# Kernel tuning notes

Hardware: AMD Instinct MI355X
Metric: run time of the kernel (lower is better)

## Reference

```python
import jax, jax.numpy as jnp
import numpy as np

SEQ, D_A, H, D_K, D_V = 4096, 2048, 16, 128, 128


def setup_inputs() -> dict:
    key = jax.random.key(0)
    ks = jax.random.split(key, 7)
    return {
        "queries": jax.random.normal(ks[0], (SEQ, D_A), dtype=jnp.float32),
        "keys":    jax.random.normal(ks[1], (SEQ, D_A), dtype=jnp.float32),
        "values":  jax.random.normal(ks[2], (SEQ, D_A), dtype=jnp.float32),
        "Eq": jax.random.normal(ks[3], (H, D_A, D_K), dtype=jnp.float32),
        "Ek": jax.random.normal(ks[4], (H, D_A, D_K), dtype=jnp.float32),
        "Ev": jax.random.normal(ks[5], (H, D_A, D_V), dtype=jnp.float32),
        "W_out": jax.random.normal(ks[6], (H * D_V, D_A), dtype=jnp.float32),
    }


def reference(queries, keys, values, Eq, Ek, Ev, W_out):
    # Per-head projections: [seq, d_a] x [h, d_a, d] -> [h, seq, d]
    Q = jnp.einsum("sd,hdk->hsk", queries, Eq)
    K = jnp.einsum("sd,hdk->hsk", keys, Ek)
    V = jnp.einsum("sd,hdv->hsv", values, Ev)
    scale = 1.0 / D_K  # faithful to source: 1/d_k, not 1/sqrt(d_k)
    dots = jnp.einsum("hqk,hsk->hqs", Q, K) * scale  # [h, seq, seq]
    attn = jax.nn.softmax(dots, axis=-1)  # dropout p=0 -> identity
    out = jnp.einsum("hqs,hsv->hqv", attn, V)  # [h, seq, d_v]
    # concat heads along last dim: [seq, h*d_v]
    A = jnp.transpose(out, (1, 0, 2)).reshape(SEQ, H * D_V)
    return A @ W_out  # [seq, d_a]
```

## Files before the change

kernel.cpp:

```cpp
#include <hip/hip_runtime.h>

typedef unsigned short u16;
typedef __attribute__((ext_vector_type(4)))  float  f32x4;
typedef __attribute__((ext_vector_type(16))) float  f32x16;
typedef __attribute__((ext_vector_type(4)))  float  float4v;
typedef __attribute__((ext_vector_type(4)))  unsigned short u16x4;
typedef __attribute__((ext_vector_type(8)))  unsigned short u16x8;
typedef __attribute__((ext_vector_type(8)))  short s16x8;
typedef __attribute__((ext_vector_type(4)))  unsigned int u32x4;

#define SEQ 4096
#define DA  2048
#define NH  16
#define DKV 128

__device__ __forceinline__ u16 f2bf(float f) {
    unsigned u = __builtin_bit_cast(unsigned, f);
    u += 0x7FFFu + ((u >> 16) & 1u);
    return (u16)(u >> 16);
}
__device__ __forceinline__ float bf2f(u16 h) {
    return __builtin_bit_cast(float, (unsigned)h << 16);
}
__device__ __forceinline__ f32x4 mfma16(u16x8 a, u16x8 b, f32x4 c) {
    return __builtin_amdgcn_mfma_f32_16x16x32_bf16(
        __builtin_bit_cast(s16x8, a), __builtin_bit_cast(s16x8, b), c, 0, 0, 0);
}
__device__ __forceinline__ f32x16 mfma32(u16x8 a, u16x8 b, f32x16 c) {
    return __builtin_amdgcn_mfma_f32_32x32x16_bf16(
        __builtin_bit_cast(s16x8, a), __builtin_bit_cast(s16x8, b), c, 0, 0, 0);
}
__device__ __forceinline__ unsigned cvtpk(float lo, float hi) {
    unsigned r;
    asm("v_cvt_pk_bf16_f32 %0, %1, %2" : "=v"(r) : "v"(lo), "v"(hi));
    return r;
}
__device__ __forceinline__ void gld16(const u16* g, u16* l) {
    __builtin_amdgcn_global_load_lds(
        (const __attribute__((address_space(1))) unsigned int*)g,
        (__attribute__((address_space(3))) unsigned int*)l, 16, 0, 0);
}
__device__ __forceinline__ char* ldsp(void* base, int row, int bcol, int rowbytes) {
    int off = row * rowbytes + bcol;
    off ^= (row & 7) << 4;
    return (char*)base + off;
}
__device__ __forceinline__ char* ldsp256(void* base, int row, int bcol) {
    int off = row * 256 + bcol;
    off ^= (row & 15) << 4;
    return (char*)base + off;
}

__global__ void transpose_split_k(const float* __restrict__ in, u16* __restrict__ oh,
                                  u16* __restrict__ ol, int R, int C) {
    __shared__ float tile[32][33];
    int b  = blockIdx.z;
    int r0 = blockIdx.x * 32, c0 = blockIdx.y * 32;
    const float* src = in + (size_t)b * R * C;
    int t = threadIdx.x;
    {
        int cl = t & 31, r = t >> 5;
        for (int i = 0; i < 4; ++i)
            tile[r + 8 * i][cl] = src[(size_t)(r0 + r + 8 * i) * C + (c0 + cl)];
    }
    __syncthreads();
    int rl = t & 31, c = t >> 5;
    size_t obase = (size_t)b * R * C;
    for (int i = 0; i < 4; ++i) {
        int cw = c + 8 * i;
        float x = tile[rl][cw];
        u16 h = f2bf(x);
        size_t o = obase + (size_t)(c0 + cw) * R + (r0 + rl);
        oh[o] = h;
        if (ol) ol[o] = f2bf(x - bf2f(h));
    }
}

__global__ void split_cvt_k(const float* __restrict__ in, u16* __restrict__ oh,
                            u16* __restrict__ ol, float scale, int n) {
    int stride = gridDim.x * 256 * 4;
    for (int i = (blockIdx.x * 256 + threadIdx.x) * 4; i < n; i += stride) {
        float4v v = *(const float4v*)(in + i);
        u16x4 hv, lv;
#pragma unroll
        for (int j = 0; j < 4; ++j) {
            float x = v[j] * scale;
            u16 hh = f2bf(x);
            hv[j] = hh;
            lv[j] = f2bf(x - bf2f(hh));
        }
        *(u16x4*)(oh + i) = hv;
        if (ol) *(u16x4*)(ol + i) = lv;
    }
}

template <int MODE>
__global__ void __launch_bounds__(256, 2) proj2_k(const u16* __restrict__ ASh,
                                                  const u16* __restrict__ ASl,
                                                  const u16* __restrict__ BTh,
                                                  const u16* __restrict__ BTl,
                                                  u16* __restrict__ Oh,
                                                  u16* __restrict__ Ol) {
    __shared__ u16 sAh[128 * 64];
    __shared__ u16 sBh[128 * 64];
    __shared__ u16 sAl[MODE ? 128 * 64 : 8];
    __shared__ u16 sBl[MODE ? 128 * 64 : 8];

    int t = threadIdx.x;
    int h = blockIdx.y;
    int bm0 = blockIdx.x * 128;
    int lane = t & 63, w = t >> 6, wr = w >> 1, wc = w & 1;
    int g = lane >> 4, c = lane & 15;

    int rin = lane >> 3;
    int cg  = (lane & 7) ^ rin;

    f32x4 acc[4][4] = {};

    for (int k0 = 0; k0 < DA; k0 += 64) {
        __syncthreads();
#pragma unroll
        for (int j = 0; j < 4; ++j) {
            int chunk = w * 4 + j;
            int r = chunk * 8 + rin;
            size_t ga = (size_t)(bm0 + r) * DA + k0 + cg * 8;
            size_t gb = ((size_t)h * 128 + r) * DA + k0 + cg * 8;
            gld16(ASh + ga, &sAh[chunk * 512]);
            gld16(BTh + gb, &sBh[chunk * 512]);
            if (MODE) {
                gld16(ASl + ga, &sAl[chunk * 512]);
                gld16(BTl + gb, &sBl[chunk * 512]);
            }
        }
        __syncthreads();

        for (int kc = 0; kc < 2; ++kc) {
            int kb = (kc * 32 + g * 8) * 2;
            u16x8 ah[4], al[4], bh[4], bl[4];
            for (int m = 0; m < 4; ++m) {
                int row = wr * 64 + m * 16 + c;
                ah[m] = *(u16x8*)ldsp(sAh, row, kb, 128);
                if (MODE) al[m] = *(u16x8*)ldsp(sAl, row, kb, 128);
            }
            for (int n = 0; n < 4; ++n) {
                int row = wc * 64 + n * 16 + c;
                bh[n] = *(u16x8*)ldsp(sBh, row, kb, 128);
                if (MODE) bl[n] = *(u16x8*)ldsp(sBl, row, kb, 128);
            }
            for (int m = 0; m < 4; ++m)
                for (int n = 0; n < 4; ++n) {
                    acc[m][n] = mfma16(ah[m], bh[n], acc[m][n]);
                    if (MODE) {
                        acc[m][n] = mfma16(ah[m], bl[n], acc[m][n]);
                        acc[m][n] = mfma16(al[m], bh[n], acc[m][n]);
                    }
                }
        }
    }

    for (int m = 0; m < 4; ++m)
        for (int n = 0; n < 4; ++n) {
            int col  = wc * 64 + n * 16 + c;
            int row0 = bm0 + wr * 64 + m * 16 + g * 4;
            if (MODE == 0) {
                u16x4 pv;
                for (int j = 0; j < 4; ++j) pv[j] = f2bf(acc[m][n][j]);
                *(u16x4*)(Oh + ((size_t)h * DKV + col) * SEQ + row0) = pv;
            } else {
                for (int j = 0; j < 4; ++j) {
                    float v = acc[m][n][j];
                    u16 hh = f2bf(v);
                    size_t o = ((size_t)h * SEQ + row0 + j) * DKV + col;
                    Oh[o] = hh;
                    Ol[o] = f2bf(v - bf2f(hh));
                }
            }
        }
}

__global__ void __launch_bounds__(512, 1) attn_k(const u16* __restrict__ QH,
                                                 const u16* __restrict__ QL,
                                                 const u16* __restrict__ KH,
                                                 const u16* __restrict__ KL,
                                                 const u16* __restrict__ VT,
                                                 u16* __restrict__ Abuf) {
    __shared__ u16 sKh[2][64 * 128];
    __shared__ u16 sKl[2][64 * 128];
    __shared__ u16 sV [2][64 * 128];

    int t = threadIdx.x, lane = t & 63, w = t >> 6;
    int bid = blockIdx.x;
    int h  = (bid & 7) + 8 * ((bid >> 3) & 1);
    int q0 = (bid >> 4) * 256;
    int c = lane & 31, hi = lane >> 5;
    int qrow = q0 + w * 32 + c;

    u16x8 qh[8], ql[8];
    {
        size_t base = ((size_t)h * SEQ + qrow) * DKV + hi * 8;
#pragma unroll
        for (int dc = 0; dc < 8; ++dc) {
            qh[dc] = *(const u16x8*)(QH + base + dc * 16);
            ql[dc] = *(const u16x8*)(QL + base + dc * 16);
        }
    }

    f32x16 o[4] = {};
    float mrun = -3e38f, lrun = 0.f;

    const size_t kroot = (size_t)h * SEQ * DKV;
    const size_t vroot = (size_t)h * DKV * SEQ;

    auto stage = [&](int kv, int b) {
        const u16* khp = KH + kroot + (size_t)kv * DKV;
        const u16* klp = KL + kroot + (size_t)kv * DKV;
        const u16* vtp = VT + vroot + kv;
#pragma unroll
        for (int j = 0; j < 2; ++j) {
            int ci = w * 2 + j;
            int rK = ci * 4 + (lane >> 4);
            int cK = (lane & 15) ^ (rK & 15);
            gld16(khp + rK * DKV + cK * 8, &sKh[b][ci * 512]);
            gld16(klp + rK * DKV + cK * 8, &sKl[b][ci * 512]);
            int vd = ((cK >> 3) << 6) + rK;
            gld16(vtp + (size_t)vd * SEQ + (cK & 7) * 8, &sV[b][ci * 512]);
        }
    };

    stage(0, 0);
    const int NT = SEQ / 64;
    for (int it = 0; it < NT; ++it) {
        int b = it & 1;
        __syncthreads();
        if (it + 1 < NT) stage((it + 1) * 64, b ^ 1);

        f32x16 s[2] = {};
        __builtin_amdgcn_s_setprio(1);
#pragma unroll
        for (int kt = 0; kt < 2; ++kt) {
#pragma unroll
            for (int dc = 0; dc < 8; ++dc) {
                u16x8 kh = *(u16x8*)ldsp256(sKh[b], kt * 32 + c, dc * 32 + hi * 16);
                u16x8 kl = *(u16x8*)ldsp256(sKl[b], kt * 32 + c, dc * 32 + hi * 16);
                s[kt] = mfma32(kh, qh[dc], s[kt]);
                s[kt] = mfma32(kl, qh[dc], s[kt]);
                s[kt] = mfma32(kh, ql[dc], s[kt]);
            }
        }
        __builtin_amdgcn_s_setprio(0);

        float vmax = s[0][0];
#pragma unroll
        for (int r = 1; r < 16; ++r) vmax = fmaxf(vmax, s[0][r]);
#pragma unroll
        for (int r = 0; r < 16; ++r) vmax = fmaxf(vmax, s[1][r]);
        vmax = fmaxf(vmax, __shfl_xor(vmax, 32));
        if (!__all(vmax <= mrun + 8.0f)) {
            float mnew = fmaxf(mrun, vmax);
            float corr = __expf(mrun - mnew);
            mrun = mnew;
            lrun *= corr;
#pragma unroll
            for (int vt = 0; vt < 4; ++vt)
#pragma unroll
                for (int r = 0; r < 16; ++r) o[vt][r] *= corr;
        }
        float rs = 0.f;
#pragma unroll
        for (int kt = 0; kt < 2; ++kt)
#pragma unroll
            for (int r = 0; r < 16; ++r) {
                float p = __expf(s[kt][r] - mrun);
                s[kt][r] = p;
                rs += p;
            }
        rs += __shfl_xor(rs, 32);
        lrun += rs;

#pragma unroll
        for (int kt = 0; kt < 2; ++kt) {
            unsigned wv[8], xw[8];
#pragma unroll
            for (int i = 0; i < 8; ++i) wv[i] = cvtpk(s[kt][2 * i], s[kt][2 * i + 1]);
#pragma unroll
            for (int i = 0; i < 8; ++i) xw[i] = (unsigned)__shfl_xor((int)wv[i], 32);
            __builtin_amdgcn_s_setprio(1);
#pragma unroll
            for (int kc = 0; kc < 2; ++kc) {
                u32x4 pw;
                pw[0] = hi ? xw[4 * kc + 2] : wv[4 * kc + 0];
                pw[1] = hi ? xw[4 * kc + 3] : wv[4 * kc + 1];
                pw[2] = hi ? wv[4 * kc + 2] : xw[4 * kc + 0];
                pw[3] = hi ? wv[4 * kc + 3] : xw[4 * kc + 1];
                u16x8 pf = __builtin_bit_cast(u16x8, pw);
#pragma unroll
                for (int vt = 0; vt < 4; ++vt) {
                    int v = vt * 32 + c;
                    u16x8 vf = *(u16x8*)ldsp256(sV[b], v & 63,
                                                ((v >> 6) << 7) + kt * 64 + kc * 32 + hi * 16);
                    o[vt] = mfma32(vf, pf, o[vt]);
                }
            }
            __builtin_amdgcn_s_setprio(0);
        }
    }

    float inv = 1.0f / lrun;
#pragma unroll
    for (int vt = 0; vt < 4; ++vt)
#pragma unroll
        for (int rg = 0; rg < 4; ++rg) {
            u16x4 pv;
#pragma unroll
            for (int j = 0; j < 4; ++j) pv[j] = f2bf(o[vt][rg * 4 + j] * inv);
            *(u16x4*)(Abuf + (size_t)qrow * (NH * DKV) + h * DKV + vt * 32 + rg * 8 + hi * 4) = pv;
        }
}

__global__ void __launch_bounds__(256, 2) gemm_out_k(const u16* __restrict__ Abuf,
                                                     const u16* __restrict__ WT,
                                                     float* __restrict__ out) {
    __shared__ u16 sA[128 * 64];
    __shared__ u16 sB[128 * 64];
    int t = threadIdx.x, lane = t & 63, w = t >> 6, wr = w >> 1, wc = w & 1;
    int g = lane >> 4, c = lane & 15;
    int bm0 = blockIdx.x * 128, bn0 = blockIdx.y * 128;
    int rin = lane >> 3;
    int cg  = (lane & 7) ^ rin;
    f32x4 acc[4][4] = {};

    for (int k0 = 0; k0 < DA; k0 += 64) {
        __syncthreads();
#pragma unroll
        for (int j = 0; j < 4; ++j) {
            int chunk = w * 4 + j;
            int r = chunk * 8 + rin;
            gld16(Abuf + (size_t)(bm0 + r) * DA + k0 + cg * 8, &sA[chunk * 512]);
            gld16(WT   + (size_t)(bn0 + r) * DA + k0 + cg * 8, &sB[chunk * 512]);
        }
        __syncthreads();

        for (int kc = 0; kc < 2; ++kc) {
            int kb = (kc * 32 + g * 8) * 2;
            u16x8 af[4], bfq[4];
            for (int m = 0; m < 4; ++m) af[m]  = *(u16x8*)ldsp(sA, wr * 64 + m * 16 + c, kb, 128);
            for (int n = 0; n < 4; ++n) bfq[n] = *(u16x8*)ldsp(sB, wc * 64 + n * 16 + c, kb, 128);
            for (int m = 0; m < 4; ++m)
                for (int n = 0; n < 4; ++n)
                    acc[m][n] = mfma16(af[m], bfq[n], acc[m][n]);
        }
    }
    for (int m = 0; m < 4; ++m)
        for (int n = 0; n < 4; ++n) {
            int row0 = bm0 + wr * 64 + m * 16 + g * 4;
            int col  = bn0 + wc * 64 + n * 16 + c;
            for (int j = 0; j < 4; ++j)
                out[(size_t)(row0 + j) * DA + col] = acc[m][n][j];
        }
}

extern "C" void kernel_launch(void* const* d_in, const int* in_sizes, int n_in,
                              void* d_out, int out_size, void* d_ws, size_t ws_size,
                              hipStream_t stream) {
    const float* queries = (const float*)d_in[0];
    const float* keys    = (const float*)d_in[1];
    const float* values  = (const float*)d_in[2];
    const float* Eq      = (const float*)d_in[3];
    const float* Ek      = (const float*)d_in[4];
    const float* Ev      = (const float*)d_in[5];
    const float* Wout    = (const float*)d_in[6];
    float* out = (float*)d_out;

    const size_t PROJ = (size_t)NH * SEQ * DKV;
    const size_t TSZ  = (size_t)DA * DA;
    const size_t ASZ  = (size_t)SEQ * DA;
    u16* p  = (u16*)d_ws;
    u16* QH = p; p += PROJ;
    u16* QL = p; p += PROJ;
    u16* KH = p; p += PROJ;
    u16* KL = p; p += PROJ;
    u16* VT = p; p += PROJ;
    u16* AB = p; p += (size_t)SEQ * NH * DKV;
    u16* TH = p; p += TSZ;
    u16* TL = p; p += TSZ;
    u16* Sh = p; p += ASZ;
    u16* Sl = p; p += ASZ;

    dim3 tgE(DA / 32, DKV / 32, NH);
    dim3 tgW(DA / 32, DA / 32, 1);
    dim3 pg(SEQ / 128, NH);
    const int NELEM = SEQ * DA;

    transpose_split_k<<<tgE, 256, 0, stream>>>(Eq, TH, TL, DA, DKV);
    split_cvt_k<<<2048, 256, 0, stream>>>(queries, Sh, Sl, 1.0f / 128.0f, NELEM);
    proj2_k<2><<<pg, 256, 0, stream>>>(Sh, Sl, TH, TL, QH, QL);
    transpose_split_k<<<tgE, 256, 0, stream>>>(Ek, TH, TL, DA, DKV);
    split_cvt_k<<<2048, 256, 0, stream>>>(keys, Sh, Sl, 1.0f, NELEM);
    proj2_k<1><<<pg, 256, 0, stream>>>(Sh, Sl, TH, TL, KH, KL);
    transpose_split_k<<<tgE, 256, 0, stream>>>(Ev, TH, nullptr, DA, DKV);
    split_cvt_k<<<2048, 256, 0, stream>>>(values, Sh, nullptr, 1.0f, NELEM);
    proj2_k<0><<<pg, 256, 0, stream>>>(Sh, nullptr, TH, nullptr, VT, nullptr);
    transpose_split_k<<<tgW, 256, 0, stream>>>(Wout, TH, nullptr, DA, DA);
    attn_k<<<dim3(SEQ / 256 * NH), 512, 0, stream>>>(QH, QL, KH, KL, VT, AB);
    gemm_out_k<<<dim3(SEQ / 128, DA / 128), 256, 0, stream>>>(AB, TH, out);
}
```

Baseline: 576.2 us.

## Double-buffer LDS tiles in projection and output GEMM kernels

Both the projection GEMM and the output GEMM now use two LDS buffers and issue the next tile's global-to-LDS loads before computing on the current tile. This overlaps memory latency with MFMA work and drops one barrier per iteration. In the projection kernel the K-step is halved to 32 so LDS use stays within budget, and a new 64-byte-row XOR swizzle is added to match. The cost is more loop iterations and barriers in the projection kernel. There is also a risk that the wait on the async global_load_lds is not explicit, so correctness depends on the compiler inserting the right waitcnt before the barrier.

```diff
diff --git a/kernel.cpp b/kernel.cpp
--- a/kernel.cpp
+++ b/kernel.cpp
@@ -48,6 +48,11 @@
 __device__ __forceinline__ char* ldsp256(void* base, int row, int bcol) {
     int off = row * 256 + bcol;
     off ^= (row & 15) << 4;
+    return (char*)base + off;
+}
+__device__ __forceinline__ char* ldsp64B(void* base, int row, int bcol) {
+    int off = row * 64 + bcol;
+    off ^= ((row ^ (row >> 2)) & 3) << 4;
     return (char*)base + off;
 }
 
@@ -101,10 +106,10 @@
                                                   const u16* __restrict__ BTl,
                                                   u16* __restrict__ Oh,
                                                   u16* __restrict__ Ol) {
-    __shared__ u16 sAh[128 * 64];
-    __shared__ u16 sBh[128 * 64];
-    __shared__ u16 sAl[MODE ? 128 * 64 : 8];
-    __shared__ u16 sBl[MODE ? 128 * 64 : 8];
+    __shared__ u16 sAh[2][128 * 32];
+    __shared__ u16 sBh[2][128 * 32];
+    __shared__ u16 sAl[2][MODE ? 128 * 32 : 8];
+    __shared__ u16 sBl[2][MODE ? 128 * 32 : 8];
 
     int t = threadIdx.x;
     int h = blockIdx.y;
@@ -112,50 +117,52 @@
     int lane = t & 63, w = t >> 6, wr = w >> 1, wc = w & 1;
     int g = lane >> 4, c = lane & 15;
 
-    int rin = lane >> 3;
-    int cg  = (lane & 7) ^ rin;
-
     f32x4 acc[4][4] = {};
 
-    for (int k0 = 0; k0 < DA; k0 += 64) {
-        __syncthreads();
-#pragma unroll
-        for (int j = 0; j < 4; ++j) {
-            int chunk = w * 4 + j;
-            int r = chunk * 8 + rin;
+    auto stage = [&](int k0, int b) {
+#pragma unroll
+        for (int j = 0; j < 2; ++j) {
+            int ci = w * 2 + j;
+            int r  = ci * 16 + (lane >> 2);
+            int cg = (lane & 3) ^ ((r ^ (r >> 2)) & 3);
             size_t ga = (size_t)(bm0 + r) * DA + k0 + cg * 8;
             size_t gb = ((size_t)h * 128 + r) * DA + k0 + cg * 8;
-            gld16(ASh + ga, &sAh[chunk * 512]);
-            gld16(BTh + gb, &sBh[chunk * 512]);
+            gld16(ASh + ga, &sAh[b][ci * 512]);
+            gld16(BTh + gb, &sBh[b][ci * 512]);
             if (MODE) {
-                gld16(ASl + ga, &sAl[chunk * 512]);
-                gld16(BTl + gb, &sBl[chunk * 512]);
-            }
-        }
+                gld16(ASl + ga, &sAl[b][ci * 512]);
+                gld16(BTl + gb, &sBl[b][ci * 512]);
+            }
+        }
+    };
+
+    stage(0, 0);
+    const int NK = DA / 32;
+    for (int ks = 0; ks < NK; ++ks) {
+        int b = ks & 1;
         __syncthreads();
-
-        for (int kc = 0; kc < 2; ++kc) {
-            int kb = (kc * 32 + g * 8) * 2;
-            u16x8 ah[4], al[4], bh[4], bl[4];
-            for (int m = 0; m < 4; ++m) {
-                int row = wr * 64 + m * 16 + c;
-                ah[m] = *(u16x8*)ldsp(sAh, row, kb, 128);
-                if (MODE) al[m] = *(u16x8*)ldsp(sAl, row, kb, 128);
-            }
+        if (ks + 1 < NK) stage((ks + 1) * 32, b ^ 1);
+
+        int kb = g * 16;
+        u16x8 ah[4], al[4], bh[4], bl[4];
+        for (int m = 0; m < 4; ++m) {
+            int row = wr * 64 + m * 16 + c;
+            ah[m] = *(u16x8*)ldsp64B(sAh[b], row, kb);
+            if (MODE) al[m] = *(u16x8*)ldsp64B(sAl[b], row, kb);
+        }
+        for (int n = 0; n < 4; ++n) {
+            int row = wc * 64 + n * 16 + c;
+            bh[n] = *(u16x8*)ldsp64B(sBh[b], row, kb);
+            if (MODE) bl[n] = *(u16x8*)ldsp64B(sBl[b], row, kb);
+        }
+        for (int m = 0; m < 4; ++m)
             for (int n = 0; n < 4; ++n) {
-                int row = wc * 64 + n * 16 + c;
-                bh[n] = *(u16x8*)ldsp(sBh, row, kb, 128);
-                if (MODE) bl[n] = *(u16x8*)ldsp(sBl, row, kb, 128);
-            }
-            for (int m = 0; m < 4; ++m)
-                for (int n = 0; n < 4; ++n) {
-                    acc[m][n] = mfma16(ah[m], bh[n], acc[m][n]);
-                    if (MODE) {
-                        acc[m][n] = mfma16(ah[m], bl[n], acc[m][n]);
-                        acc[m][n] = mfma16(al[m], bh[n], acc[m][n]);
-                    }
+                acc[m][n] = mfma16(ah[m], bh[n], acc[m][n]);
+                if (MODE) {
+                    acc[m][n] = mfma16(ah[m], bl[n], acc[m][n]);
+                    acc[m][n] = mfma16(al[m], bh[n], acc[m][n]);
                 }
-        }
+            }
     }
 
     for (int m = 0; m < 4; ++m)
@@ -320,8 +327,8 @@
 __global__ void __launch_bounds__(256, 2) gemm_out_k(const u16* __restrict__ Abuf,
                                                      const u16* __restrict__ WT,
                                                      float* __restrict__ out) {
-    __shared__ u16 sA[128 * 64];
-    __shared__ u16 sB[128 * 64];
+    __shared__ u16 sA[2][128 * 64];
+    __shared__ u16 sB[2][128 * 64];
     int t = threadIdx.x, lane = t & 63, w = t >> 6, wr = w >> 1, wc = w & 1;
     int g = lane >> 4, c = lane & 15;
     int bm0 = blockIdx.x * 128, bn0 = blockIdx.y * 128;
@@ -329,22 +336,28 @@
     int cg  = (lane & 7) ^ rin;
     f32x4 acc[4][4] = {};
 
-    for (int k0 = 0; k0 < DA; k0 += 64) {
-        __syncthreads();
+    auto stage = [&](int k0, int b) {
 #pragma unroll
         for (int j = 0; j < 4; ++j) {
             int chunk = w * 4 + j;
             int r = chunk * 8 + rin;
-            gld16(Abuf + (size_t)(bm0 + r) * DA + k0 + cg * 8, &sA[chunk * 512]);
-            gld16(WT   + (size_t)(bn0 + r) * DA + k0 + cg * 8, &sB[chunk * 512]);
-        }
+            gld16(Abuf + (size_t)(bm0 + r) * DA + k0 + cg * 8, &sA[b][chunk * 512]);
+            gld16(WT   + (size_t)(bn0 + r) * DA + k0 + cg * 8, &sB[b][chunk * 512]);
+        }
+    };
+
+    stage(0, 0);
+    const int NK = DA / 64;
+    for (int ks = 0; ks < NK; ++ks) {
+        int b = ks & 1;
         __syncthreads();
+        if (ks + 1 < NK) stage((ks + 1) * 64, b ^ 1);
 
         for (int kc = 0; kc < 2; ++kc) {
             int kb = (kc * 32 + g * 8) * 2;
             u16x8 af[4], bfq[4];
-            for (int m = 0; m < 4; ++m) af[m]  = *(u16x8*)ldsp(sA, wr * 64 + m * 16 + c, kb, 128);
-            for (int n = 0; n < 4; ++n) bfq[n] = *(u16x8*)ldsp(sB, wc * 64 + n * 16 + c, kb, 128);
+            for (int m = 0; m < 4; ++m) af[m]  = *(u16x8*)ldsp(sA[b], wr * 64 + m * 16 + c, kb, 128);
+            for (int n = 0; n < 4; ++n) bfq[n] = *(u16x8*)ldsp(sB[b], wc * 64 + n * 16 + c, kb, 128);
             for (int m = 0; m < 4; ++m)
                 for (int n = 0; n < 4; ++n)
                     acc[m][n] = mfma16(af[m], bfq[n], acc[m][n]);
```

Result: slower. 611.6 us (+6.2%).

## Pre-tile V into MFMA fragment layout and load directly from global to registers

Applied to the files above, without the earlier changes.

The projection kernel now writes V in a blocked layout that matches the MFMA B-fragment order for each 64-key tile. The attention kernel drops the V shared-memory buffer and async staging, and instead loads V fragments with coalesced 16-byte global loads straight into registers at the start of each iteration. This removes LDS traffic and LDS capacity for V, but exposes global-load latency inside the loop without double-buffering and raises register pressure by 16 vector registers of fragments. The projection's V output also changes from vector stores to scattered scalar stores.

```diff
diff --git a/kernel.cpp b/kernel.cpp
--- a/kernel.cpp
+++ b/kernel.cpp
@@ -163,9 +163,16 @@
             int col  = wc * 64 + n * 16 + c;
             int row0 = bm0 + wr * 64 + m * 16 + g * 4;
             if (MODE == 0) {
-                u16x4 pv;
-                for (int j = 0; j < 4; ++j) pv[j] = f2bf(acc[m][n][j]);
-                *(u16x4*)(Oh + ((size_t)h * DKV + col) * SEQ + row0) = pv;
+                for (int j = 0; j < 4; ++j) {
+                    int s = row0 + j;
+                    size_t o = (size_t)h * (SEQ * DKV)
+                             + (size_t)(s >> 6) * 8192
+                             + (size_t)((s >> 4) & 3) * 2048
+                             + (size_t)(col >> 5) * 512
+                             + (size_t)(((s >> 3) & 1) * 32 + (col & 31)) * 8
+                             + (s & 7);
+                    Oh[o] = f2bf(acc[m][n][j]);
+                }
             } else {
                 for (int j = 0; j < 4; ++j) {
                     float v = acc[m][n][j];
@@ -186,7 +193,6 @@
                                                  u16* __restrict__ Abuf) {
     __shared__ u16 sKh[2][64 * 128];
     __shared__ u16 sKl[2][64 * 128];
-    __shared__ u16 sV [2][64 * 128];
 
     int t = threadIdx.x, lane = t & 63, w = t >> 6;
     int bid = blockIdx.x;
@@ -209,12 +215,11 @@
     float mrun = -3e38f, lrun = 0.f;
 
     const size_t kroot = (size_t)h * SEQ * DKV;
-    const size_t vroot = (size_t)h * DKV * SEQ;
+    const u16* vroot = VT + (size_t)h * DKV * SEQ;
 
     auto stage = [&](int kv, int b) {
         const u16* khp = KH + kroot + (size_t)kv * DKV;
         const u16* klp = KL + kroot + (size_t)kv * DKV;
-        const u16* vtp = VT + vroot + kv;
 #pragma unroll
         for (int j = 0; j < 2; ++j) {
             int ci = w * 2 + j;
@@ -222,8 +227,6 @@
             int cK = (lane & 15) ^ (rK & 15);
             gld16(khp + rK * DKV + cK * 8, &sKh[b][ci * 512]);
             gld16(klp + rK * DKV + cK * 8, &sKl[b][ci * 512]);
-            int vd = ((cK >> 3) << 6) + rK;
-            gld16(vtp + (size_t)vd * SEQ + (cK & 7) * 8, &sV[b][ci * 512]);
         }
     };
 
@@ -232,6 +235,16 @@
     for (int it = 0; it < NT; ++it) {
         int b = it & 1;
         __syncthreads();
+
+        const u16* vtile = vroot + (size_t)it * 8192;
+        u16x8 va[8], vb[8];
+#pragma unroll
+        for (int i = 0; i < 8; ++i) {
+            int kc = i >> 2, vt = i & 3;
+            va[i] = *(const u16x8*)(vtile + (0 + kc) * 2048 + vt * 512 + lane * 8);
+            vb[i] = *(const u16x8*)(vtile + (2 + kc) * 2048 + vt * 512 + lane * 8);
+        }
+
         if (it + 1 < NT) stage((it + 1) * 64, b ^ 1);
 
         f32x16 s[2] = {};
@@ -294,12 +307,9 @@
                 pw[3] = hi ? wv[4 * kc + 3] : xw[4 * kc + 1];
                 u16x8 pf = __builtin_bit_cast(u16x8, pw);
 #pragma unroll
-                for (int vt = 0; vt < 4; ++vt) {
-                    int v = vt * 32 + c;
-                    u16x8 vf = *(u16x8*)ldsp256(sV[b], v & 63,
-                                                ((v >> 6) << 7) + kt * 64 + kc * 32 + hi * 16);
-                    o[vt] = mfma32(vf, pf, o[vt]);
-                }
+                for (int vt = 0; vt < 4; ++vt)
+                    o[vt] = mfma32(kt == 0 ? va[kc * 4 + vt] : vb[kc * 4 + vt],
+                                   pf, o[vt]);
             }
             __builtin_amdgcn_s_setprio(0);
         }
```

After: 654.1 us. 13.5% more time.
